# Performance work log

Measured on AMD Instinct MI355X. Metric: run time of the kernel, lower is better.

The kernel has to match this reference:

```python
import jax, jax.numpy as jnp
import numpy as np
import math

NUM_HEADS = 8
LN_EPS = 1e-5


def layer_norm(x, g, b):
    mu = x.mean(-1, keepdims=True)
    var = ((x - mu) ** 2).mean(-1, keepdims=True)
    return (x - mu) * jax.lax.rsqrt(var + LN_EPS) * g + b


def typed_linear(x, W, types):
    # x: [E, in], W: [R, in, out], types: [E] int -> [E, out]
    out = jnp.zeros((x.shape[0], W.shape[-1]), x.dtype)
    for r in range(W.shape[0]):  # small fixed relation count
        out = out + jnp.where((types == r)[:, None], x @ W[r], 0.0)
    return out


def setup_inputs() -> dict:
    key = jax.random.key(0)
    ks = jax.random.split(key, 20)
    N, M, E = 50000, 10000, 100000
    in_dim, e_dim, out_dim, td = 128, 32, 128, 32
    R, T = 8, 4
    inp = {
        'src_h': jax.random.normal(ks[0], (N, in_dim), jnp.float32),
        'src_tw': jax.random.normal(ks[1], (N, td), jnp.float32),
        'src_tb': jax.random.normal(ks[2], (N, td), jnp.float32),
        'edge_h': jax.random.normal(ks[3], (E, e_dim), jnp.float32),
        'date': jax.random.uniform(ks[4], (E,), jnp.float32),
        'src_idx': jax.random.randint(ks[5], (E,), 0, N, jnp.int32),
        'dst_idx': jax.random.randint(ks[6], (E,), 0, M, jnp.int32),
        'etype': jax.random.randint(ks[7], (E,), 0, R, jnp.int32),
        'ntype': jax.random.randint(ks[8], (M,), 0, T, jnp.int32),
    }
    def w(k, shape):
        return jax.random.normal(k, shape, jnp.float32) / math.sqrt(shape[-2])
    inp['Wq'] = w(ks[9], (R, in_dim, out_dim))
    inp['Wk'] = w(ks[10], (R, in_dim + e_dim, out_dim))
    inp['Wv'] = w(ks[11], (R, in_dim + e_dim, out_dim))
    inp['Wa'] = w(ks[12], (T, out_dim, out_dim))
    inp['h_bias'] = jnp.zeros((T, out_dim), jnp.float32)
    inp['skip'] = jnp.ones((T,), jnp.float32)
    inp['src_ln_g'] = jnp.ones((in_dim + e_dim,), jnp.float32)
    inp['src_ln_b'] = jnp.zeros((in_dim + e_dim,), jnp.float32)
    inp['dst_ln_g'] = jnp.ones((in_dim,), jnp.float32)
    inp['dst_ln_b'] = jnp.zeros((in_dim,), jnp.float32)
    return inp


def reference(src_h, src_tw, src_tb, edge_h, date, src_idx, dst_idx, etype, ntype,
              Wq, Wk, Wv, Wa, h_bias, skip, src_ln_g, src_ln_b, dst_ln_g, dst_ln_b):
    M = ntype.shape[0]
    out_dim = Wq.shape[-1]
    H = NUM_HEADS
    hs = out_dim // H
    td = src_tw.shape[-1]
    t = date[:, None]  # [E,1]

    # gather src / dst node data per edge (dst nodes are first M src rows)
    h_s, tw_s, tb_s = src_h[src_idx], src_tw[src_idx], src_tb[src_idx]
    h_d, tw_d, tb_d = src_h[dst_idx], src_tw[dst_idx], src_tb[dst_idx]

    # time2vec modulation of the first td channels
    dia_s = jnp.concatenate([jnp.sin(tw_s * t + tb_s) * h_s[:, :td], h_s[:, td:]], -1)
    dia_d = jnp.concatenate([jnp.sin(tw_d * t + tb_d) * h_d[:, :td], h_d[:, td:]], -1)
    dia_s = jnp.concatenate([dia_s, edge_h], -1)  # [E, in_dim+e_dim]

    # pre_norm
    dia_s = layer_norm(dia_s, src_ln_g, src_ln_b)
    dia_d = layer_norm(dia_d, dst_ln_g, dst_ln_b)

    q = typed_linear(dia_d, Wq, etype).reshape(-1, H, hs)
    k = typed_linear(dia_s, Wk, etype).reshape(-1, H, hs)
    v = typed_linear(dia_s, Wv, etype).reshape(-1, H, hs)

    a = (q * k).sum(-1) / math.sqrt(out_dim)  # [E, H]

    # edge_softmax: segment softmax over destination nodes
    amax = jax.lax.stop_gradient(jax.ops.segment_max(a, dst_idx, num_segments=M))
    ex = jnp.exp(a - amax[dst_idx])
    denom = jax.ops.segment_sum(ex, dst_idx, num_segments=M)
    alpha = ex / denom[dst_idx]  # [E, H]

    # weighted scatter-sum aggregation
    m = (v * alpha[..., None]).reshape(-1, out_dim)  # [E, out_dim]
    h = jax.ops.segment_sum(m, dst_idx, num_segments=M)  # [M, out_dim]

    h = h + h_bias[ntype]
    gate = jax.nn.sigmoid(skip[ntype])[:, None]
    h = typed_linear(h, Wa, ntype)  # dropout is identity at eval
    dst_h = src_h[:M]
    return h * gate + dst_h * (1.0 - gate)
```

## Files before the change

kernel.cpp:

```cpp
#include <hip/hip_runtime.h>


typedef __attribute__((ext_vector_type(8))) short short8;
typedef __attribute__((ext_vector_type(4))) float f32x4;

__device__ __forceinline__ unsigned short f2bf(float f){
  union { float f; unsigned u; } x; x.f = f;
  unsigned r = x.u + 0x7FFFu + ((x.u >> 16) & 1u);
  return (unsigned short)(r >> 16);
}
__device__ __forceinline__ float bf2f(unsigned short b){
  union { unsigned u; float f; } x; x.u = ((unsigned)b) << 16;
  return x.f;
}
__device__ __forceinline__ float wred(float v){
  #pragma unroll
  for(int i=1;i<64;i<<=1) v += __shfl_xor(v, i);
  return v;
}


__global__ void k_zero(int* __restrict__ p, int n){
  int i = blockIdx.x*256 + threadIdx.x;
  if(i < n) p[i] = 0;
}

__global__ __launch_bounds__(256) void k_hist(
    const int* __restrict__ etype, const int* __restrict__ dst_idx,
    const int* __restrict__ ntype,
    int* cnt_e, int* cnt_d, int* cnt_n, int E, int M){
  __shared__ int le[8], ln[4];
  int tid = threadIdx.x;
  if(tid < 8) le[tid] = 0;
  if(tid < 4) ln[tid] = 0;
  __syncthreads();
  int g = blockIdx.x*256 + tid;
  if(g < E){ atomicAdd(&le[etype[g]], 1); atomicAdd(&cnt_d[dst_idx[g]], 1); }
  if(g < M){ atomicAdd(&ln[ntype[g]], 1); }
  __syncthreads();
  if(tid < 8 && le[tid]) atomicAdd(&cnt_e[tid], le[tid]);
  if(tid < 4 && ln[tid]) atomicAdd(&cnt_n[tid], ln[tid]);
}

__global__ __launch_bounds__(1024) void k_scan(const int* __restrict__ cnt_e, int* off_e,
                                               const int* __restrict__ cnt_n, int* off_n,
                                               const int* __restrict__ cnt_d, int* off_d, int M){
  __shared__ int part[1024];
  int tid = threadIdx.x;
  if(tid == 0){
    int s = 0;
    for(int i=0;i<8;i++){ off_e[i]=s; s+=cnt_e[i]; } off_e[8]=s;
    s = 0;
    for(int i=0;i<4;i++){ off_n[i]=s; s+=cnt_n[i]; } off_n[4]=s;
  }
  int per = (M + 1023) >> 10;
  int s = 0;
  for(int j=0;j<per;j++){ int idx = tid*per + j; if(idx < M) s += cnt_d[idx]; }
  part[tid] = s; __syncthreads();
  for(int o=1;o<1024;o<<=1){
    int v = (tid >= o) ? part[tid-o] : 0;
    __syncthreads();
    part[tid] += v;
    __syncthreads();
  }
  int run = (tid == 0) ? 0 : part[tid-1];
  for(int j=0;j<per;j++){
    int idx = tid*per + j;
    if(idx < M){ off_d[idx] = run; run += cnt_d[idx]; }
  }
  if(tid == 1023) off_d[M] = run;
}

__global__ __launch_bounds__(256) void k_scatter(
    const int* __restrict__ etype, const int* __restrict__ dst_idx,
    const int* __restrict__ ntype,
    const int* __restrict__ off_e, int* cur_e,
    const int* __restrict__ off_d, int* cur_d,
    const int* __restrict__ off_n, int* cur_n,
    int* eperm, int* dstlist, int* nperm, int* npos, int E, int M){
  __shared__ int lcnt[8], lbase[8], lnc[4], lnb[4];
  int tid = threadIdx.x;
  if(tid < 8) lcnt[tid] = 0;
  if(tid < 4) lnc[tid] = 0;
  __syncthreads();
  int g = blockIdx.x*256 + tid;
  int r = 0, lrank = 0, t = 0, nrank = 0;
  bool inE = (g < E), inM = (g < M);
  if(inE){ r = etype[g]; lrank = atomicAdd(&lcnt[r], 1); }
  if(inM){ t = ntype[g]; nrank = atomicAdd(&lnc[t], 1); }
  __syncthreads();
  if(tid < 8 && lcnt[tid]) lbase[tid] = atomicAdd(&cur_e[tid], lcnt[tid]);
  if(tid < 4 && lnc[tid])  lnb[tid]   = atomicAdd(&cur_n[tid], lnc[tid]);
  __syncthreads();
  if(inE){
    int p = off_e[r] + lbase[r] + lrank;
    eperm[p] = g;
    int d = dst_idx[g];
    int q = off_d[d] + atomicAdd(&cur_d[d], 1);
    dstlist[q] = p;
  }
  if(inM){
    int np = off_n[t] + lnb[t] + nrank;
    npos[g] = np;
    nperm[np] = g;
  }
}

__global__ void k_convw(const float* __restrict__ Wq, const float* __restrict__ Wk,
                        const float* __restrict__ Wv, const float* __restrict__ Wa,
                        unsigned short* Wq_t, unsigned short* Wk_t,
                        unsigned short* Wv_t, unsigned short* Wa_t){
  int tid = blockIdx.x*256 + threadIdx.x;
  if(tid < 131072){
    int r = tid >> 14, rem = tid & 16383, i = rem >> 7, o = rem & 127;
    Wq_t[(r<<14) + (o<<7) + i] = f2bf(Wq[tid]);
  } else if(tid < 294912){
    int u = tid - 131072;
    int r = u / 20480, rem = u - r*20480, i = rem >> 7, o = rem & 127;
    Wk_t[r*20480 + o*160 + i] = f2bf(Wk[u]);
  } else if(tid < 458752){
    int u = tid - 294912;
    int r = u / 20480, rem = u - r*20480, i = rem >> 7, o = rem & 127;
    Wv_t[r*20480 + o*160 + i] = f2bf(Wv[u]);
  } else if(tid < 524288){
    int u = tid - 458752;
    int r = u >> 14, rem = u & 16383, i = rem >> 7, o = rem & 127;
    Wa_t[(r<<14) + (o<<7) + i] = f2bf(Wa[u]);
  }
}

__global__ __launch_bounds__(256) void k_prep(
  const float* __restrict__ src_h, const float* __restrict__ src_tw, const float* __restrict__ src_tb,
  const float* __restrict__ edge_h, const float* __restrict__ date,
  const int* __restrict__ src_idx, const int* __restrict__ dst_idx, const int* __restrict__ eperm,
  const float* __restrict__ g_s, const float* __restrict__ b_s,
  const float* __restrict__ g_d, const float* __restrict__ b_d,
  unsigned short* __restrict__ dia_s, unsigned short* __restrict__ dia_d, int E)
{
  int p = blockIdx.x*4 + (threadIdx.x >> 6);
  if(p >= E) return;
  int lane = threadIdx.x & 63;
  int e = eperm[p];
  float t = date[e];
  int s = src_idx[e], d = dst_idx[e];
  {
    float h0 = src_h[(size_t)s*128 + lane];
    float h1 = src_h[(size_t)s*128 + 64 + lane];
    float x0 = h0, x2 = 0.f;
    if(lane < 32){
      x0 = __sinf(src_tw[s*32 + lane]*t + src_tb[s*32 + lane]) * h0;
      x2 = edge_h[(size_t)e*32 + lane];
    }
    float x1 = h1;
    float mu = wred(x0 + x1 + x2) * (1.f/160.f);
    float d0 = x0-mu, d1 = x1-mu, d2 = (lane<32) ? (x2-mu) : 0.f;
    float var = wred(d0*d0 + d1*d1 + d2*d2) * (1.f/160.f);
    float sc = rsqrtf(var + 1e-5f);
    size_t bo = (size_t)p*160;
    dia_s[bo + lane]      = f2bf(d0*sc*g_s[lane]      + b_s[lane]);
    dia_s[bo + 64 + lane] = f2bf(d1*sc*g_s[64+lane]   + b_s[64+lane]);
    if(lane < 32)
      dia_s[bo + 128 + lane] = f2bf(d2*sc*g_s[128+lane] + b_s[128+lane]);
  }
  {
    float h0 = src_h[(size_t)d*128 + lane];
    float h1 = src_h[(size_t)d*128 + 64 + lane];
    float x0 = (lane < 32) ? __sinf(src_tw[d*32+lane]*t + src_tb[d*32+lane]) * h0 : h0;
    float x1 = h1;
    float mu = wred(x0 + x1) * (1.f/128.f);
    float d0 = x0-mu, d1 = x1-mu;
    float var = wred(d0*d0 + d1*d1) * (1.f/128.f);
    float sc = rsqrtf(var + 1e-5f);
    size_t bo = (size_t)p*128;
    dia_d[bo + lane]      = f2bf(d0*sc*g_d[lane]    + b_d[lane]);
    dia_d[bo + 64 + lane] = f2bf(d1*sc*g_d[64+lane] + b_d[64+lane]);
  }
}

__device__ __forceinline__ void gemm64(
  const unsigned short* __restrict__ A, int lda,
  const unsigned short* __restrict__ Wg, int Kd,
  unsigned short* __restrict__ Bt, f32x4* acc, int tid)
{
  int lane = tid & 63, w = tid >> 6, m = lane & 15, quad = lane >> 4;
  #pragma unroll
  for(int i=0;i<8;i++) acc[i] = (f32x4){0.f,0.f,0.f,0.f};
  for(int k0=0; k0<Kd; k0+=32){
    __syncthreads();
    #pragma unroll
    for(int j=0;j<2;j++){
      int idx = j*256 + tid;
      int n = idx >> 2, qc = idx & 3;
      *(int4*)(Bt + n*40 + qc*8) = *(const int4*)(Wg + (size_t)n*Kd + k0 + qc*8);
    }
    __syncthreads();
    short8 b0 = *(const short8*)(Bt + (w*32 +      m)*40 + quad*8);
    short8 b1 = *(const short8*)(Bt + (w*32 + 16 + m)*40 + quad*8);
    #pragma unroll
    for(int rt=0; rt<4; rt++){
      short8 af = *(const short8*)(A + (rt*16 + m)*lda + k0 + quad*8);
      acc[rt*2+0] = __builtin_amdgcn_mfma_f32_16x16x32_bf16(af, b0, acc[rt*2+0], 0,0,0);
      acc[rt*2+1] = __builtin_amdgcn_mfma_f32_16x16x32_bf16(af, b1, acc[rt*2+1], 0,0,0);
    }
  }
}

__global__ __launch_bounds__(256) void k_qkv(
  const unsigned short* __restrict__ dia_d, const unsigned short* __restrict__ dia_s,
  const unsigned short* __restrict__ Wq_t, const unsigned short* __restrict__ Wk_t,
  const unsigned short* __restrict__ Wv_t,
  const int* __restrict__ cnt_e, const int* __restrict__ off_e,
  float* __restrict__ abuf, unsigned short* __restrict__ vbuf)
{
  __shared__ unsigned short Ad[64*136];
  __shared__ unsigned short As[64*168];
  __shared__ unsigned short Bt[128*40];
  int bid = blockIdx.x;
  int r = -1, tl0 = 0, accT = 0;
  #pragma unroll
  for(int i=0;i<8;i++){
    int n = cnt_e[i], tt = (n + 63) >> 6;
    if(r < 0 && bid < accT + tt){ r = i; tl0 = bid - accT; }
    accT += tt;
  }
  if(r < 0) return;
  int row0 = off_e[r] + tl0*64;
  int nv = min(64, cnt_e[r] - tl0*64);
  int tid = threadIdx.x;
  {
    int4 z = make_int4(0,0,0,0);
    #pragma unroll
    for(int it=0; it<4; it++){
      int idx = it*256 + tid, row = idx >> 4, c = idx & 15;
      int4 v = z;
      if(row < nv) v = *(const int4*)(dia_d + (size_t)(row0+row)*128 + c*8);
      *(int4*)(Ad + row*136 + c*8) = v;
    }
    #pragma unroll
    for(int it=0; it<5; it++){
      int idx = it*256 + tid, row = idx/20, c = idx%20;
      int4 v = z;
      if(row < nv) v = *(const int4*)(dia_s + (size_t)(row0+row)*160 + c*8);
      *(int4*)(As + row*168 + c*8) = v;
    }
  }
  int lane = tid & 63, w = tid >> 6, m = lane & 15, quad = lane >> 4;
  f32x4 q[8], kk[8], vv[8];
  gemm64(Ad, 136, Wq_t + r*16384, 128, Bt, q,  tid);
  gemm64(As, 168, Wk_t + r*20480, 160, Bt, kk, tid);
  const float inv = 0.08838834764831845f;
  #pragma unroll
  for(int rt=0; rt<4; rt++)
  #pragma unroll
  for(int ct=0; ct<2; ct++){
    #pragma unroll
    for(int reg=0; reg<4; reg++){
      float s = q[rt*2+ct][reg] * kk[rt*2+ct][reg];
      s += __shfl_xor(s,1); s += __shfl_xor(s,2); s += __shfl_xor(s,4); s += __shfl_xor(s,8);
      int row = rt*16 + quad*4 + reg;
      if(m == 0 && row < nv) abuf[(size_t)(row0+row)*8 + w*2 + ct] = s * inv;
    }
  }
  gemm64(As, 168, Wv_t + r*20480, 160, Bt, vv, tid);
  #pragma unroll
  for(int rt=0; rt<4; rt++)
  #pragma unroll
  for(int ct=0; ct<2; ct++)
  #pragma unroll
  for(int reg=0; reg<4; reg++){
    int row = rt*16 + quad*4 + reg;
    if(row < nv)
      vbuf[(size_t)(row0+row)*128 + w*32 + ct*16 + m] = f2bf(vv[rt*2+ct][reg]);
  }
}

__global__ __launch_bounds__(128) void k_aggr(
  const float* __restrict__ abuf, const unsigned short* __restrict__ vbuf,
  const int* __restrict__ dstlist, const int* __restrict__ off_d,
  const int* __restrict__ npos, const int* __restrict__ ntype,
  const float* __restrict__ h_bias, unsigned short* __restrict__ hpre)
{
  int d = blockIdx.x, tid = threadIdx.x;
  int o0 = off_d[d], cnt = off_d[d+1] - o0;
  __shared__ float den[8];
  if(tid < 8) den[tid] = 0.f;
  __syncthreads();
  for(int idx = tid; idx < cnt*8; idx += 128){
    int i = idx >> 3, h = idx & 7;
    float ex = __expf(abuf[(size_t)dstlist[o0+i]*8 + h]);
    atomicAdd(&den[h], ex);
  }
  __syncthreads();
  int h = tid >> 4;
  float dh = den[h];
  float rd = (dh > 0.f) ? (1.f/dh) : 0.f;
  float acc = 0.f;
  for(int i=0; i<cnt; i++){
    int p = dstlist[o0+i];
    float al = __expf(abuf[(size_t)p*8 + h]) * rd;
    acc += al * bf2f(vbuf[(size_t)p*128 + tid]);
  }
  int t = ntype[d];
  acc += h_bias[t*128 + tid];
  hpre[(size_t)npos[d]*128 + tid] = f2bf(acc);
}

__global__ __launch_bounds__(256) void k_final(
  const unsigned short* __restrict__ hpre, const unsigned short* __restrict__ Wa_t,
  const int* __restrict__ cnt_n, const int* __restrict__ off_n, const int* __restrict__ nperm,
  const float* __restrict__ skip, const float* __restrict__ src_h, float* __restrict__ out)
{
  __shared__ unsigned short Ah[64*136];
  __shared__ unsigned short Bt[128*40];
  int bid = blockIdx.x;
  int r = -1, tl0 = 0, accT = 0;
  #pragma unroll
  for(int i=0;i<4;i++){
    int n = cnt_n[i], tt = (n + 63) >> 6;
    if(r < 0 && bid < accT + tt){ r = i; tl0 = bid - accT; }
    accT += tt;
  }
  if(r < 0) return;
  int row0 = off_n[r] + tl0*64;
  int nv = min(64, cnt_n[r] - tl0*64);
  float gate = 1.f / (1.f + __expf(-skip[r]));
  int tid = threadIdx.x;
  int4 z = make_int4(0,0,0,0);
  #pragma unroll
  for(int it=0; it<4; it++){
    int idx = it*256 + tid, row = idx >> 4, c = idx & 15;
    int4 v = z;
    if(row < nv) v = *(const int4*)(hpre + (size_t)(row0+row)*128 + c*8);
    *(int4*)(Ah + row*136 + c*8) = v;
  }
  f32x4 acc[8];
  gemm64(Ah, 136, Wa_t + r*16384, 128, Bt, acc, tid);
  int lane = tid & 63, w = tid >> 6, m = lane & 15, quad = lane >> 4;
  #pragma unroll
  for(int rt=0; rt<4; rt++)
  #pragma unroll
  for(int ct=0; ct<2; ct++)
  #pragma unroll
  for(int reg=0; reg<4; reg++){
    int row = rt*16 + quad*4 + reg;
    if(row < nv){
      int dd = nperm[row0+row];
      int col = w*32 + ct*16 + m;
      out[(size_t)dd*128 + col] = acc[rt*2+ct][reg]*gate + src_h[(size_t)dd*128 + col]*(1.f - gate);
    }
  }
}

extern "C" void kernel_launch(void* const* d_in, const int* in_sizes, int n_in,
                              void* d_out, int out_size, void* d_ws, size_t ws_size,
                              hipStream_t stream)
{
  const float* src_h  = (const float*)d_in[0];
  const float* src_tw = (const float*)d_in[1];
  const float* src_tb = (const float*)d_in[2];
  const float* edge_h = (const float*)d_in[3];
  const float* date   = (const float*)d_in[4];
  const int*   src_idx= (const int*)d_in[5];
  const int*   dst_idx= (const int*)d_in[6];
  const int*   etype  = (const int*)d_in[7];
  const int*   ntype  = (const int*)d_in[8];
  const float* Wq     = (const float*)d_in[9];
  const float* Wk     = (const float*)d_in[10];
  const float* Wv     = (const float*)d_in[11];
  const float* Wa     = (const float*)d_in[12];
  const float* h_bias = (const float*)d_in[13];
  const float* skip   = (const float*)d_in[14];
  const float* g_s    = (const float*)d_in[15];
  const float* b_s    = (const float*)d_in[16];
  const float* g_d    = (const float*)d_in[17];
  const float* b_d    = (const float*)d_in[18];
  float* out = (float*)d_out;

  const int E = in_sizes[4];
  const int M = in_sizes[8];

  char* base = (char*)d_ws;
  size_t off = 0;
  auto alloc = [&](size_t bytes)->char*{
    off = (off + 255) & ~(size_t)255;
    char* p = base + off; off += bytes; return p;
  };
  int* cnt_e = (int*)alloc((size_t)(24 + 2*M)*4);
  int* cur_e = cnt_e + 8;
  int* cnt_n = cur_e + 8;
  int* cur_n = cnt_n + 4;
  int* cnt_d = cur_n + 4;
  int* cur_d = cnt_d + M;
  const int nzero = 24 + 2*M;
  int* off_e = (int*)alloc(9*4);
  int* off_n = (int*)alloc(5*4);
  int* off_d = (int*)alloc((size_t)(M+1)*4);
  int* eperm   = (int*)alloc((size_t)E*4);
  int* dstlist = (int*)alloc((size_t)E*4);
  int* nperm   = (int*)alloc((size_t)M*4);
  int* npos    = (int*)alloc((size_t)M*4);
  unsigned short* Wq_t = (unsigned short*)alloc((size_t)8*128*128*2);
  unsigned short* Wk_t = (unsigned short*)alloc((size_t)8*160*128*2);
  unsigned short* Wv_t = (unsigned short*)alloc((size_t)8*160*128*2);
  unsigned short* Wa_t = (unsigned short*)alloc((size_t)4*128*128*2);
  unsigned short* dia_d = (unsigned short*)alloc((size_t)E*128*2);
  unsigned short* dia_s = (unsigned short*)alloc((size_t)E*160*2);
  unsigned short* vbuf  = (unsigned short*)alloc((size_t)E*128*2);
  unsigned short* hpre  = (unsigned short*)alloc((size_t)M*128*2);
  float* abuf = (float*)alloc((size_t)E*8*4);

  k_zero<<<dim3((nzero+255)/256), dim3(256), 0, stream>>>(cnt_e, nzero);
  k_hist<<<dim3((E+255)/256), dim3(256), 0, stream>>>(etype, dst_idx, ntype, cnt_e, cnt_d, cnt_n, E, M);
  k_scan<<<dim3(1), dim3(1024), 0, stream>>>(cnt_e, off_e, cnt_n, off_n, cnt_d, off_d, M);
  k_scatter<<<dim3((E+255)/256), dim3(256), 0, stream>>>(etype, dst_idx, ntype,
      off_e, cur_e, off_d, cur_d, off_n, cur_n, eperm, dstlist, nperm, npos, E, M);
  k_convw<<<dim3(2048), dim3(256), 0, stream>>>(Wq, Wk, Wv, Wa, Wq_t, Wk_t, Wv_t, Wa_t);
  k_prep<<<dim3((E+3)/4), dim3(256), 0, stream>>>(src_h, src_tw, src_tb, edge_h, date,
      src_idx, dst_idx, eperm, g_s, b_s, g_d, b_d, dia_s, dia_d, E);
  k_qkv<<<dim3(E/64 + 9), dim3(256), 0, stream>>>(dia_d, dia_s, Wq_t, Wk_t, Wv_t,
      cnt_e, off_e, abuf, vbuf);
  k_aggr<<<dim3(M), dim3(128), 0, stream>>>(abuf, vbuf, dstlist, off_d, npos, ntype, h_bias, hpre);
  k_final<<<dim3(M/64 + 5), dim3(256), 0, stream>>>(hpre, Wa_t, cnt_n, off_n, nperm, skip, src_h, out);
}
```

Baseline: 290.0 us.

## Pack edge records, vectorize prep, enlarge GEMM tiles, precompute exp, slim aggregation

Result: slower. 409.8 us (+41.3%).

```diff
diff --git a/kernel.cpp b/kernel.cpp
--- a/kernel.cpp
+++ b/kernel.cpp
@@ -12,11 +12,6 @@
 __device__ __forceinline__ float bf2f(unsigned short b){
   union { unsigned u; float f; } x; x.u = ((unsigned)b) << 16;
   return x.f;
-}
-__device__ __forceinline__ float wred(float v){
-  #pragma unroll
-  for(int i=1;i<64;i<<=1) v += __shfl_xor(v, i);
-  return v;
 }
 
 
@@ -72,12 +67,13 @@
 }
 
 __global__ __launch_bounds__(256) void k_scatter(
-    const int* __restrict__ etype, const int* __restrict__ dst_idx,
+    const int* __restrict__ etype, const int* __restrict__ src_idx,
+    const int* __restrict__ dst_idx, const float* __restrict__ date,
     const int* __restrict__ ntype,
     const int* __restrict__ off_e, int* cur_e,
     const int* __restrict__ off_d, int* cur_d,
     const int* __restrict__ off_n, int* cur_n,
-    int* eperm, int* dstlist, int* nperm, int* npos, int E, int M){
+    int4* __restrict__ recs, int* dstlist, int* nperm, int* npos, int E, int M){
   __shared__ int lcnt[8], lbase[8], lnc[4], lnb[4];
   int tid = threadIdx.x;
   if(tid < 8) lcnt[tid] = 0;
@@ -94,8 +90,11 @@
   __syncthreads();
   if(inE){
     int p = off_e[r] + lbase[r] + lrank;
-    eperm[p] = g;
-    int d = dst_idx[g];
+    int4 rec;
+    rec.x = src_idx[g]; rec.y = dst_idx[g]; rec.z = g;
+    rec.w = __float_as_int(date[g]);
+    recs[p] = rec;
+    int d = rec.y;
     int q = off_d[d] + atomicAdd(&cur_d[d], 1);
     dstlist[q] = p;
   }
@@ -131,8 +130,7 @@
 
 __global__ __launch_bounds__(256) void k_prep(
   const float* __restrict__ src_h, const float* __restrict__ src_tw, const float* __restrict__ src_tb,
-  const float* __restrict__ edge_h, const float* __restrict__ date,
-  const int* __restrict__ src_idx, const int* __restrict__ dst_idx, const int* __restrict__ eperm,
+  const float* __restrict__ edge_h, const int4* __restrict__ recs,
   const float* __restrict__ g_s, const float* __restrict__ b_s,
   const float* __restrict__ g_d, const float* __restrict__ b_d,
   unsigned short* __restrict__ dia_s, unsigned short* __restrict__ dia_d, int E)
@@ -140,51 +138,74 @@
   int p = blockIdx.x*4 + (threadIdx.x >> 6);
   if(p >= E) return;
   int lane = threadIdx.x & 63;
-  int e = eperm[p];
-  float t = date[e];
-  int s = src_idx[e], d = dst_idx[e];
+  int4 rec = recs[p];
+  int s = rec.x, d = rec.y, e = rec.z;
+  float t = __int_as_float(rec.w);
+
   {
-    float h0 = src_h[(size_t)s*128 + lane];
-    float h1 = src_h[(size_t)s*128 + 64 + lane];
-    float x0 = h0, x2 = 0.f;
-    if(lane < 32){
-      x0 = __sinf(src_tw[s*32 + lane]*t + src_tb[s*32 + lane]) * h0;
-      x2 = edge_h[(size_t)e*32 + lane];
-    }
-    float x1 = h1;
-    float mu = wred(x0 + x1 + x2) * (1.f/160.f);
-    float d0 = x0-mu, d1 = x1-mu, d2 = (lane<32) ? (x2-mu) : 0.f;
-    float var = wred(d0*d0 + d1*d1 + d2*d2) * (1.f/160.f);
+    float2 h2 = *(const float2*)(src_h + (size_t)s*128 + 2*lane);
+    float x0 = h2.x, x1 = h2.y;
+    if(lane < 16){
+      float2 tw2 = *(const float2*)(src_tw + s*32 + 2*lane);
+      float2 tb2 = *(const float2*)(src_tb + s*32 + 2*lane);
+      x0 = __sinf(tw2.x*t + tb2.x) * h2.x;
+      x1 = __sinf(tw2.y*t + tb2.y) * h2.y;
+    }
+    float e0 = 0.f, e1 = 0.f;
+    if(lane >= 16 && lane < 32){
+      float2 eh = *(const float2*)(edge_h + (size_t)e*32 + 2*(lane-16));
+      e0 = eh.x; e1 = eh.y;
+    }
+    float s1 = x0+x1+e0+e1, s2 = x0*x0+x1*x1+e0*e0+e1*e1;
+    #pragma unroll
+    for(int i=1;i<64;i<<=1){ s1 += __shfl_xor(s1,i); s2 += __shfl_xor(s2,i); }
+    float mu = s1*(1.f/160.f);
+    float var = s2*(1.f/160.f) - mu*mu;
     float sc = rsqrtf(var + 1e-5f);
-    size_t bo = (size_t)p*160;
-    dia_s[bo + lane]      = f2bf(d0*sc*g_s[lane]      + b_s[lane]);
-    dia_s[bo + 64 + lane] = f2bf(d1*sc*g_s[64+lane]   + b_s[64+lane]);
-    if(lane < 32)
-      dia_s[bo + 128 + lane] = f2bf(d2*sc*g_s[128+lane] + b_s[128+lane]);
+    float2 g2 = *(const float2*)(g_s + 2*lane);
+    float2 b2 = *(const float2*)(b_s + 2*lane);
+    float o0 = (x0-mu)*sc*g2.x + b2.x;
+    float o1 = (x1-mu)*sc*g2.y + b2.y;
+    ((unsigned*)dia_s)[(size_t)p*80 + lane] = (unsigned)f2bf(o0) | ((unsigned)f2bf(o1)<<16);
+    if(lane >= 16 && lane < 32){
+      float2 g2e = *(const float2*)(g_s + 128 + 2*(lane-16));
+      float2 b2e = *(const float2*)(b_s + 128 + 2*(lane-16));
+      float q0 = (e0-mu)*sc*g2e.x + b2e.x;
+      float q1 = (e1-mu)*sc*g2e.y + b2e.y;
+      ((unsigned*)dia_s)[(size_t)p*80 + 48 + lane] = (unsigned)f2bf(q0) | ((unsigned)f2bf(q1)<<16);
+    }
   }
   {
-    float h0 = src_h[(size_t)d*128 + lane];
-    float h1 = src_h[(size_t)d*128 + 64 + lane];
-    float x0 = (lane < 32) ? __sinf(src_tw[d*32+lane]*t + src_tb[d*32+lane]) * h0 : h0;
-    float x1 = h1;
-    float mu = wred(x0 + x1) * (1.f/128.f);
-    float d0 = x0-mu, d1 = x1-mu;
-    float var = wred(d0*d0 + d1*d1) * (1.f/128.f);
+    float2 h2 = *(const float2*)(src_h + (size_t)d*128 + 2*lane);
+    float y0 = h2.x, y1 = h2.y;
+    if(lane < 16){
+      float2 tw2 = *(const float2*)(src_tw + d*32 + 2*lane);
+      float2 tb2 = *(const float2*)(src_tb + d*32 + 2*lane);
+      y0 = __sinf(tw2.x*t + tb2.x) * h2.x;
+      y1 = __sinf(tw2.y*t + tb2.y) * h2.y;
+    }
+    float s1 = y0+y1, s2 = y0*y0+y1*y1;
+    #pragma unroll
+    for(int i=1;i<64;i<<=1){ s1 += __shfl_xor(s1,i); s2 += __shfl_xor(s2,i); }
+    float mu = s1*(1.f/128.f);
+    float var = s2*(1.f/128.f) - mu*mu;
     float sc = rsqrtf(var + 1e-5f);
-    size_t bo = (size_t)p*128;
-    dia_d[bo + lane]      = f2bf(d0*sc*g_d[lane]    + b_d[lane]);
-    dia_d[bo + 64 + lane] = f2bf(d1*sc*g_d[64+lane] + b_d[64+lane]);
-  }
-}
-
-__device__ __forceinline__ void gemm64(
-  const unsigned short* __restrict__ A, int lda,
+    float2 g2 = *(const float2*)(g_d + 2*lane);
+    float2 b2 = *(const float2*)(b_d + 2*lane);
+    float o0 = (y0-mu)*sc*g2.x + b2.x;
+    float o1 = (y1-mu)*sc*g2.y + b2.y;
+    ((unsigned*)dia_d)[(size_t)p*64 + lane] = (unsigned)f2bf(o0) | ((unsigned)f2bf(o1)<<16);
+  }
+}
+
+__device__ __forceinline__ void gemm_g(
+  const unsigned short* __restrict__ A, int ld, int nv,
   const unsigned short* __restrict__ Wg, int Kd,
   unsigned short* __restrict__ Bt, f32x4* acc, int tid)
 {
   int lane = tid & 63, w = tid >> 6, m = lane & 15, quad = lane >> 4;
   #pragma unroll
-  for(int i=0;i<8;i++) acc[i] = (f32x4){0.f,0.f,0.f,0.f};
+  for(int i=0;i<16;i++) acc[i] = (f32x4){0.f,0.f,0.f,0.f};
   for(int k0=0; k0<Kd; k0+=32){
     __syncthreads();
     #pragma unroll
@@ -197,8 +218,10 @@
     short8 b0 = *(const short8*)(Bt + (w*32 +      m)*40 + quad*8);
     short8 b1 = *(const short8*)(Bt + (w*32 + 16 + m)*40 + quad*8);
     #pragma unroll
-    for(int rt=0; rt<4; rt++){
-      short8 af = *(const short8*)(A + (rt*16 + m)*lda + k0 + quad*8);
+    for(int rt=0; rt<8; rt++){
+      int row = rt*16 + m;
+      short8 af = (short8){0,0,0,0,0,0,0,0};
+      if(row < nv) af = *(const short8*)(A + (size_t)row*ld + k0 + quad*8);
       acc[rt*2+0] = __builtin_amdgcn_mfma_f32_16x16x32_bf16(af, b0, acc[rt*2+0], 0,0,0);
       acc[rt*2+1] = __builtin_amdgcn_mfma_f32_16x16x32_bf16(af, b1, acc[rt*2+1], 0,0,0);
     }
@@ -212,97 +235,82 @@
   const int* __restrict__ cnt_e, const int* __restrict__ off_e,
   float* __restrict__ abuf, unsigned short* __restrict__ vbuf)
 {
-  __shared__ unsigned short Ad[64*136];
-  __shared__ unsigned short As[64*168];
   __shared__ unsigned short Bt[128*40];
   int bid = blockIdx.x;
   int r = -1, tl0 = 0, accT = 0;
   #pragma unroll
   for(int i=0;i<8;i++){
-    int n = cnt_e[i], tt = (n + 63) >> 6;
+    int n = cnt_e[i], tt = (n + 127) >> 7;
     if(r < 0 && bid < accT + tt){ r = i; tl0 = bid - accT; }
     accT += tt;
   }
   if(r < 0) return;
-  int row0 = off_e[r] + tl0*64;
-  int nv = min(64, cnt_e[r] - tl0*64);
+  int row0 = off_e[r] + tl0*128;
+  int nv = min(128, cnt_e[r] - tl0*128);
   int tid = threadIdx.x;
-  {
-    int4 z = make_int4(0,0,0,0);
-    #pragma unroll
-    for(int it=0; it<4; it++){
-      int idx = it*256 + tid, row = idx >> 4, c = idx & 15;
-      int4 v = z;
-      if(row < nv) v = *(const int4*)(dia_d + (size_t)(row0+row)*128 + c*8);
-      *(int4*)(Ad + row*136 + c*8) = v;
-    }
-    #pragma unroll
-    for(int it=0; it<5; it++){
-      int idx = it*256 + tid, row = idx/20, c = idx%20;
-      int4 v = z;
-      if(row < nv) v = *(const int4*)(dia_s + (size_t)(row0+row)*160 + c*8);
-      *(int4*)(As + row*168 + c*8) = v;
-    }
-  }
   int lane = tid & 63, w = tid >> 6, m = lane & 15, quad = lane >> 4;
-  f32x4 q[8], kk[8], vv[8];
-  gemm64(Ad, 136, Wq_t + r*16384, 128, Bt, q,  tid);
-  gemm64(As, 168, Wk_t + r*20480, 160, Bt, kk, tid);
+  const unsigned short* Aq = dia_d + (size_t)row0*128;
+  const unsigned short* As = dia_s + (size_t)row0*160;
+
+  f32x4 qa[16], ka[16];
+  gemm_g(Aq, 128, nv, Wq_t + r*16384, 128, Bt, qa, tid);
+  gemm_g(As, 160, nv, Wk_t + r*20480, 160, Bt, ka, tid);
+
   const float inv = 0.08838834764831845f;
   #pragma unroll
-  for(int rt=0; rt<4; rt++)
+  for(int rt=0; rt<8; rt++)
   #pragma unroll
   for(int ct=0; ct<2; ct++){
     #pragma unroll
     for(int reg=0; reg<4; reg++){
-      float s = q[rt*2+ct][reg] * kk[rt*2+ct][reg];
+      float s = qa[rt*2+ct][reg] * ka[rt*2+ct][reg];
       s += __shfl_xor(s,1); s += __shfl_xor(s,2); s += __shfl_xor(s,4); s += __shfl_xor(s,8);
       int row = rt*16 + quad*4 + reg;
-      if(m == 0 && row < nv) abuf[(size_t)(row0+row)*8 + w*2 + ct] = s * inv;
-    }
-  }
-  gemm64(As, 168, Wv_t + r*20480, 160, Bt, vv, tid);
-  #pragma unroll
-  for(int rt=0; rt<4; rt++)
+      if(m == 0 && row < nv) abuf[(size_t)(row0+row)*8 + w*2 + ct] = __expf(s * inv);
+    }
+  }
+
+  gemm_g(As, 160, nv, Wv_t + r*20480, 160, Bt, qa, tid);
+  #pragma unroll
+  for(int rt=0; rt<8; rt++)
   #pragma unroll
   for(int ct=0; ct<2; ct++)
   #pragma unroll
   for(int reg=0; reg<4; reg++){
     int row = rt*16 + quad*4 + reg;
     if(row < nv)
-      vbuf[(size_t)(row0+row)*128 + w*32 + ct*16 + m] = f2bf(vv[rt*2+ct][reg]);
-  }
-}
-
-__global__ __launch_bounds__(128) void k_aggr(
+      vbuf[(size_t)(row0+row)*128 + w*32 + ct*16 + m] = f2bf(qa[rt*2+ct][reg]);
+  }
+}
+
+__global__ __launch_bounds__(64) void k_aggr(
   const float* __restrict__ abuf, const unsigned short* __restrict__ vbuf,
   const int* __restrict__ dstlist, const int* __restrict__ off_d,
   const int* __restrict__ npos, const int* __restrict__ ntype,
   const float* __restrict__ h_bias, unsigned short* __restrict__ hpre)
 {
-  int d = blockIdx.x, tid = threadIdx.x;
+  int d = blockIdx.x, lane = threadIdx.x;
   int o0 = off_d[d], cnt = off_d[d+1] - o0;
-  __shared__ float den[8];
-  if(tid < 8) den[tid] = 0.f;
-  __syncthreads();
-  for(int idx = tid; idx < cnt*8; idx += 128){
-    int i = idx >> 3, h = idx & 7;
-    float ex = __expf(abuf[(size_t)dstlist[o0+i]*8 + h]);
-    atomicAdd(&den[h], ex);
-  }
-  __syncthreads();
-  int h = tid >> 4;
-  float dh = den[h];
+  float denp = 0.f;
+  for(int i = (lane>>3); i < cnt; i += 8)
+    denp += abuf[(size_t)dstlist[o0+i]*8 + (lane & 7)];
+  denp += __shfl_xor(denp, 8); denp += __shfl_xor(denp, 16); denp += __shfl_xor(denp, 32);
+  float dh = __shfl(denp, lane >> 3);
   float rd = (dh > 0.f) ? (1.f/dh) : 0.f;
-  float acc = 0.f;
+  float a0 = 0.f, a1 = 0.f;
+  const unsigned* vb = (const unsigned*)vbuf;
   for(int i=0; i<cnt; i++){
     int p = dstlist[o0+i];
-    float al = __expf(abuf[(size_t)p*8 + h]) * rd;
-    acc += al * bf2f(vbuf[(size_t)p*128 + tid]);
+    float al = abuf[(size_t)p*8 + (lane>>3)] * rd;
+    unsigned v2 = vb[(size_t)p*64 + lane];
+    a0 += al * bf2f((unsigned short)(v2 & 0xffff));
+    a1 += al * bf2f((unsigned short)(v2 >> 16));
   }
   int t = ntype[d];
-  acc += h_bias[t*128 + tid];
-  hpre[(size_t)npos[d]*128 + tid] = f2bf(acc);
+  a0 += h_bias[t*128 + 2*lane];
+  a1 += h_bias[t*128 + 2*lane + 1];
+  ((unsigned*)hpre)[(size_t)npos[d]*64 + lane] =
+      (unsigned)f2bf(a0) | ((unsigned)f2bf(a1) << 16);
 }
 
 __global__ __launch_bounds__(256) void k_final(
@@ -310,34 +318,25 @@
   const int* __restrict__ cnt_n, const int* __restrict__ off_n, const int* __restrict__ nperm,
   const float* __restrict__ skip, const float* __restrict__ src_h, float* __restrict__ out)
 {
-  __shared__ unsigned short Ah[64*136];
   __shared__ unsigned short Bt[128*40];
   int bid = blockIdx.x;
   int r = -1, tl0 = 0, accT = 0;
   #pragma unroll
   for(int i=0;i<4;i++){
-    int n = cnt_n[i], tt = (n + 63) >> 6;
+    int n = cnt_n[i], tt = (n + 127) >> 7;
     if(r < 0 && bid < accT + tt){ r = i; tl0 = bid - accT; }
     accT += tt;
   }
   if(r < 0) return;
-  int row0 = off_n[r] + tl0*64;
-  int nv = min(64, cnt_n[r] - tl0*64);
+  int row0 = off_n[r] + tl0*128;
+  int nv = min(128, cnt_n[r] - tl0*128);
   float gate = 1.f / (1.f + __expf(-skip[r]));
   int tid = threadIdx.x;
-  int4 z = make_int4(0,0,0,0);
-  #pragma unroll
-  for(int it=0; it<4; it++){
-    int idx = it*256 + tid, row = idx >> 4, c = idx & 15;
-    int4 v = z;
-    if(row < nv) v = *(const int4*)(hpre + (size_t)(row0+row)*128 + c*8);
-    *(int4*)(Ah + row*136 + c*8) = v;
-  }
-  f32x4 acc[8];
-  gemm64(Ah, 136, Wa_t + r*16384, 128, Bt, acc, tid);
   int lane = tid & 63, w = tid >> 6, m = lane & 15, quad = lane >> 4;
-  #pragma unroll
-  for(int rt=0; rt<4; rt++)
+  f32x4 acc[16];
+  gemm_g(hpre + (size_t)row0*128, 128, nv, Wa_t + r*16384, 128, Bt, acc, tid);
+  #pragma unroll
+  for(int rt=0; rt<8; rt++)
   #pragma unroll
   for(int ct=0; ct<2; ct++)
   #pragma unroll
@@ -395,7 +394,7 @@
   int* off_e = (int*)alloc(9*4);
   int* off_n = (int*)alloc(5*4);
   int* off_d = (int*)alloc((size_t)(M+1)*4);
-  int* eperm   = (int*)alloc((size_t)E*4);
+  int4* recs   = (int4*)alloc((size_t)E*16);
   int* dstlist = (int*)alloc((size_t)E*4);
   int* nperm   = (int*)alloc((size_t)M*4);
   int* npos    = (int*)alloc((size_t)M*4);
@@ -412,13 +411,13 @@
   k_zero<<<dim3((nzero+255)/256), dim3(256), 0, stream>>>(cnt_e, nzero);
   k_hist<<<dim3((E+255)/256), dim3(256), 0, stream>>>(etype, dst_idx, ntype, cnt_e, cnt_d, cnt_n, E, M);
   k_scan<<<dim3(1), dim3(1024), 0, stream>>>(cnt_e, off_e, cnt_n, off_n, cnt_d, off_d, M);
-  k_scatter<<<dim3((E+255)/256), dim3(256), 0, stream>>>(etype, dst_idx, ntype,
-      off_e, cur_e, off_d, cur_d, off_n, cur_n, eperm, dstlist, nperm, npos, E, M);
+  k_scatter<<<dim3((E+255)/256), dim3(256), 0, stream>>>(etype, src_idx, dst_idx, date, ntype,
+      off_e, cur_e, off_d, cur_d, off_n, cur_n, recs, dstlist, nperm, npos, E, M);
   k_convw<<<dim3(2048), dim3(256), 0, stream>>>(Wq, Wk, Wv, Wa, Wq_t, Wk_t, Wv_t, Wa_t);
-  k_prep<<<dim3((E+3)/4), dim3(256), 0, stream>>>(src_h, src_tw, src_tb, edge_h, date,
-      src_idx, dst_idx, eperm, g_s, b_s, g_d, b_d, dia_s, dia_d, E);
-  k_qkv<<<dim3(E/64 + 9), dim3(256), 0, stream>>>(dia_d, dia_s, Wq_t, Wk_t, Wv_t,
+  k_prep<<<dim3((E+3)/4), dim3(256), 0, stream>>>(src_h, src_tw, src_tb, edge_h, recs,
+      g_s, b_s, g_d, b_d, dia_s, dia_d, E);
+  k_qkv<<<dim3(E/128 + 9), dim3(256), 0, stream>>>(dia_d, dia_s, Wq_t, Wk_t, Wv_t,
       cnt_e, off_e, abuf, vbuf);
-  k_aggr<<<dim3(M), dim3(128), 0, stream>>>(abuf, vbuf, dstlist, off_d, npos, ntype, h_bias, hpre);
-  k_final<<<dim3(M/64 + 5), dim3(256), 0, stream>>>(hpre, Wa_t, cnt_n, off_n, nperm, skip, src_h, out);
-}
+  k_aggr<<<dim3(M), dim3(64), 0, stream>>>(abuf, vbuf, dstlist, off_d, npos, ntype, h_bias, hpre);
+  k_final<<<dim3(M/128 + 5), dim3(256), 0, stream>>>(hpre, Wa_t, cnt_n, off_n, nperm, skip, src_h, out);
+}
```
